# Optimization experiments

Hardware: AMD Instinct MI355X
Metric: run time of the kernel (lower is better)

The kernel has to match this reference:

```python
import jax, jax.numpy as jnp
import numpy as np


def sign_ste(x):
    # torch BNN Binarize: sign() applied to .data => forward sign, backward identity (STE)
    return x + jax.lax.stop_gradient(jnp.sign(x) - x)


def setup_inputs() -> dict:
    key = jax.random.key(0)
    ks = jax.random.split(key, 5)
    B = 65536
    return {
        "x": jax.random.normal(ks[0], (B, 1, 28, 28), dtype=jnp.float32),
        "w_conv": jax.random.normal(ks[1], (3, 1, 4, 4), dtype=jnp.float32) * 0.1,
        "b_conv": jax.random.normal(ks[2], (3,), dtype=jnp.float32) * 0.1,
        "w_fc": jax.random.normal(ks[3], (10, 1875), dtype=jnp.float32) * 0.05,
        "b_fc": jax.random.normal(ks[4], (10,), dtype=jnp.float32) * 0.05,
    }


def reference(x, w_conv, b_conv, w_fc, b_fc):
    # BinarizeConv2d(1,3,4): binarize input (in_ch=1 != 3) and weights, float bias
    xb = sign_ste(x)
    wcb = sign_ste(w_conv)
    y = jax.lax.conv_general_dilated(
        xb, wcb, window_strides=(1, 1), padding="VALID",
        dimension_numbers=("NCHW", "OIHW", "NCHW"))  # [B,3,25,25]
    y = y + b_conv[None, :, None, None]
    h = y.reshape(y.shape[0], -1)  # [B,1875]
    # BinarizeLinear(1875,10): binarize input (1875 != 784) and weights
    hb = sign_ste(h)
    wfb = sign_ste(w_fc)
    out = hb @ wfb.T + b_fc  # [B,10]
    return sign_ste(out)
```

## Files before the change

### kernel.cpp

```cpp
#include <hip/hip_runtime.h>
#include <stdint.h>

#define XWORDS (65536 * 28)

__device__ __forceinline__ void FA(uint32_t a, uint32_t b, uint32_t c,
                                   uint32_t& s, uint32_t& cy) {
  uint32_t ab = a ^ b;
  s = ab ^ c;
  cy = (a & b) | (ab & c);
}

__global__ __launch_bounds__(256) void pack_kernel(
    const float* __restrict__ x, const float* __restrict__ w_fc,
    uint32_t* __restrict__ xp, uint32_t* __restrict__ wfp)
{
  int t = blockIdx.x * 256 + threadIdx.x;
  if (t < XWORDS) {
    const float4* p = (const float4*)(x + (size_t)t * 28);
    uint32_t m = 0;
    #pragma unroll
    for (int q = 0; q < 7; ++q) {
      float4 v = p[q];
      m = (m >> 1) | (__float_as_uint(v.x) & 0x80000000u);
      m = (m >> 1) | (__float_as_uint(v.y) & 0x80000000u);
      m = (m >> 1) | (__float_as_uint(v.z) & 0x80000000u);
      m = (m >> 1) | (__float_as_uint(v.w) & 0x80000000u);
    }
    xp[t] = m >> 4;
  } else {
    int s = t - XWORDS;
    if (s < 750) {
      int ci = s / 10, k = s % 10;
      uint32_t m = 0;
      #pragma unroll
      for (int j = 0; j < 25; ++j)
        m |= (__float_as_uint(w_fc[k * 1875 + ci * 25 + j]) >> 31) << j;
      wfp[ci * 12 + k] = m;
    }
  }
}

__global__ __launch_bounds__(256) void bnn_main(
    const uint32_t* __restrict__ xp, const uint32_t* __restrict__ wfp,
    const float* __restrict__ w_conv, const float* __restrict__ b_conv,
    const float* __restrict__ b_fc, float* __restrict__ out)
{
  __shared__ __align__(16) uint32_t swf[900];
  __shared__ uint32_t srows[256 * 29];
  const int tid = threadIdx.x;
  const int b = blockIdx.x * 256 + tid;

  for (int i = tid; i < 900; i += 256) swf[i] = wfp[i];

  const uint4* rp = (const uint4*)(xp + (size_t)b * 28);
  uint32_t* my = &srows[tid * 29];
  #pragma unroll
  for (int q = 0; q < 7; ++q) {
    uint4 v = rp[q];
    my[q * 4 + 0] = v.x; my[q * 4 + 1] = v.y;
    my[q * 4 + 2] = v.z; my[q * 4 + 3] = v.w;
  }
  __syncthreads();

  uint32_t wm[3][16], sbc[3];
  #pragma unroll
  for (int c = 0; c < 3; ++c) {
    #pragma unroll
    for (int uv = 0; uv < 16; ++uv)
      wm[c][uv] = (uint32_t)((int32_t)__float_as_uint(w_conv[c * 16 + uv]) >> 31);
    sbc[c] = (uint32_t)((int32_t)__float_as_uint(b_conv[c]) >> 31);
  }

  int nd[10] = {0, 0, 0, 0, 0, 0, 0, 0, 0, 0};

  for (int i = 0; i < 25; ++i) {
    uint32_t r0 = my[i], r1 = my[i + 1], r2 = my[i + 2], r3 = my[i + 3];
    #pragma unroll
    for (int c = 0; c < 3; ++c) {
      const uint32_t* W = wm[c];
      uint32_t s0, c0, s1, c1, s2, c2, s3, c3, s4, c4;
      FA( r0 ^ W[0],        (r0 ^ W[1])  >> 1, (r0 ^ W[2])  >> 2, s0, c0);
      FA((r0 ^ W[3]) >> 3,   r1 ^ W[4],        (r1 ^ W[5])  >> 1, s1, c1);
      FA((r1 ^ W[6]) >> 2,  (r1 ^ W[7])  >> 3,  r2 ^ W[8],        s2, c2);
      FA((r2 ^ W[9]) >> 1,  (r2 ^ W[10]) >> 2, (r2 ^ W[11]) >> 3, s3, c3);
      FA( r3 ^ W[12],       (r3 ^ W[13]) >> 1, (r3 ^ W[14]) >> 2, s4, c4);
      uint32_t t15 = (r3 ^ W[15]) >> 3;
      uint32_t u0, d0, u1, d1;
      FA(s0, s1, s2, u0, d0); FA(s3, s4, t15, u1, d1);
      uint32_t bb0 = u0 ^ u1, e0 = u0 & u1;
      uint32_t p0, q0, p1, q1, p2, q2;
      FA(c0, c1, c2, p0, q0); FA(c3, c4, d0, p1, q1); FA(d1, e0, p0, p2, q2);
      uint32_t bb1 = p1 ^ p2, q3 = p1 & p2;
      uint32_t r0_, r1_;
      FA(q0, q1, q2, r0_, r1_);
      uint32_t bb2 = r0_ ^ q3, r2_ = r0_ & q3;
      uint32_t bb3 = r1_ ^ r2_, bb4 = r1_ & r2_;
      uint32_t low = bb0 | bb1 | bb2;
      uint32_t neg = (bb4 | (bb3 & (low | sbc[c]))) & 0x1FFFFFFu;
      int ci = c * 25 + i;
      uint4 wA = *(const uint4*)&swf[ci * 12];
      uint4 wB = *(const uint4*)&swf[ci * 12 + 4];
      uint2 wC = *(const uint2*)&swf[ci * 12 + 8];
      nd[0] += __popc(neg ^ wA.x); nd[1] += __popc(neg ^ wA.y);
      nd[2] += __popc(neg ^ wA.z); nd[3] += __popc(neg ^ wA.w);
      nd[4] += __popc(neg ^ wB.x); nd[5] += __popc(neg ^ wB.y);
      nd[6] += __popc(neg ^ wB.z); nd[7] += __popc(neg ^ wB.w);
      nd[8] += __popc(neg ^ wC.x); nd[9] += __popc(neg ^ wC.y);
    }
  }

  float* op = out + (size_t)b * 10;
  #pragma unroll
  for (int k = 0; k < 10; k += 2) {
    float v0 = (float)(1875 - 2 * nd[k])     + b_fc[k];
    float v1 = (float)(1875 - 2 * nd[k + 1]) + b_fc[k + 1];
    float2 st;
    st.x = v0 < 0.f ? -1.f : (v0 > 0.f ? 1.f : 0.f);
    st.y = v1 < 0.f ? -1.f : (v1 > 0.f ? 1.f : 0.f);
    *(float2*)(op + k) = st;
  }
}

extern "C" void kernel_launch(void* const* d_in, const int* in_sizes, int n_in,
                              void* d_out, int out_size, void* d_ws, size_t ws_size,
                              hipStream_t stream) {
  const float* x      = (const float*)d_in[0];
  const float* w_conv = (const float*)d_in[1];
  const float* b_conv = (const float*)d_in[2];
  const float* w_fc   = (const float*)d_in[3];
  const float* b_fc   = (const float*)d_in[4];

  uint32_t* xp  = (uint32_t*)d_ws;
  uint32_t* wfp = xp + XWORDS;

  pack_kernel<<<7171, 256, 0, stream>>>(x, w_fc, xp, wfp);
  bnn_main<<<256, 256, 0, stream>>>(xp, wfp, w_conv, b_conv, b_fc, (float*)d_out);
}
```

Before: 304.3 us.

## Fuse input packing into main kernel and split conv rows across four lanes

Merges the separate pack kernel into the main kernel. Each 256-thread block now loads 64 images with coalesced float4 reads, packs their sign bits into shared memory, and rebuilds 28-bit row masks. Each image's 25 output rows are split across 4 threads, with the partial popcounts combined by xor-shuffles. This removes the packed-input round trip through global memory and the second launch, and raises the grid from 256 blocks to 1024. The cost is that every block repacks the FC weights and the shuffles add a reduction step.

```diff
diff --git a/kernel.cpp b/kernel.cpp
--- a/kernel.cpp
+++ b/kernel.cpp
@@ -1,7 +1,8 @@
 #include <hip/hip_runtime.h>
 #include <stdint.h>
 
-#define XWORDS (65536 * 28)
+#define IMB 64
+#define NBLK (65536 / IMB)
 
 __device__ __forceinline__ void FA(uint32_t a, uint32_t b, uint32_t c,
                                    uint32_t& s, uint32_t& cy) {
@@ -10,72 +11,71 @@
   cy = (a & b) | (ab & c);
 }
 
-__global__ __launch_bounds__(256) void pack_kernel(
-    const float* __restrict__ x, const float* __restrict__ w_fc,
-    uint32_t* __restrict__ xp, uint32_t* __restrict__ wfp)
-{
-  int t = blockIdx.x * 256 + threadIdx.x;
-  if (t < XWORDS) {
-    const float4* p = (const float4*)(x + (size_t)t * 28);
-    uint32_t m = 0;
-    #pragma unroll
-    for (int q = 0; q < 7; ++q) {
-      float4 v = p[q];
-      m = (m >> 1) | (__float_as_uint(v.x) & 0x80000000u);
-      m = (m >> 1) | (__float_as_uint(v.y) & 0x80000000u);
-      m = (m >> 1) | (__float_as_uint(v.z) & 0x80000000u);
-      m = (m >> 1) | (__float_as_uint(v.w) & 0x80000000u);
-    }
-    xp[t] = m >> 4;
-  } else {
-    int s = t - XWORDS;
-    if (s < 750) {
-      int ci = s / 10, k = s % 10;
-      uint32_t m = 0;
-      #pragma unroll
-      for (int j = 0; j < 25; ++j)
-        m |= (__float_as_uint(w_fc[k * 1875 + ci * 25 + j]) >> 31) << j;
-      wfp[ci * 12 + k] = m;
-    }
-  }
-}
-
-__global__ __launch_bounds__(256) void bnn_main(
-    const uint32_t* __restrict__ xp, const uint32_t* __restrict__ wfp,
-    const float* __restrict__ w_conv, const float* __restrict__ b_conv,
+__global__ __launch_bounds__(256) void bnn_fused(
+    const float* __restrict__ x, const float* __restrict__ w_conv,
+    const float* __restrict__ b_conv, const float* __restrict__ w_fc,
     const float* __restrict__ b_fc, float* __restrict__ out)
 {
+  __shared__ uint8_t  nib[IMB * 196];
+  __shared__ uint32_t srows[IMB * 29];
   __shared__ __align__(16) uint32_t swf[900];
-  __shared__ uint32_t srows[256 * 29];
   const int tid = threadIdx.x;
-  const int b = blockIdx.x * 256 + tid;
-
-  for (int i = tid; i < 900; i += 256) swf[i] = wfp[i];
-
-  const uint4* rp = (const uint4*)(xp + (size_t)b * 28);
-  uint32_t* my = &srows[tid * 29];
-  #pragma unroll
-  for (int q = 0; q < 7; ++q) {
-    uint4 v = rp[q];
-    my[q * 4 + 0] = v.x; my[q * 4 + 1] = v.y;
-    my[q * 4 + 2] = v.z; my[q * 4 + 3] = v.w;
-  }
-  __syncthreads();
 
   uint32_t wm[3][16], sbc[3];
-  #pragma unroll
+#pragma unroll
   for (int c = 0; c < 3; ++c) {
-    #pragma unroll
+#pragma unroll
     for (int uv = 0; uv < 16; ++uv)
       wm[c][uv] = (uint32_t)((int32_t)__float_as_uint(w_conv[c * 16 + uv]) >> 31);
     sbc[c] = (uint32_t)((int32_t)__float_as_uint(b_conv[c]) >> 31);
   }
 
-  int nd[10] = {0, 0, 0, 0, 0, 0, 0, 0, 0, 0};
+  for (int s = tid; s < 750; s += 256) {
+    int ci = s / 10, k = s - ci * 10;
+    const float* wr = w_fc + k * 1875 + ci * 25;
+    uint32_t m = 0;
+#pragma unroll
+    for (int j = 0; j < 25; ++j)
+      m |= (__float_as_uint(wr[j]) >> 31) << j;
+    swf[ci * 12 + k] = m;
+  }
 
-  for (int i = 0; i < 25; ++i) {
+  const float4* xv = (const float4*)(x + (size_t)blockIdx.x * (IMB * 784));
+#pragma unroll 4
+  for (int q = 0; q < 49; ++q) {
+    int idx = q * 256 + tid;
+    float4 v = xv[idx];
+    uint32_t n = (__float_as_uint(v.x) >> 31)
+               | ((__float_as_uint(v.y) >> 31) << 1)
+               | ((__float_as_uint(v.z) >> 31) << 2)
+               | ((__float_as_uint(v.w) >> 31) << 3);
+    nib[idx] = (uint8_t)n;
+  }
+  __syncthreads();
+
+#pragma unroll
+  for (int q = 0; q < 7; ++q) {
+    int r = q * 256 + tid;
+    const uint8_t* p = &nib[r * 7];
+    uint32_t m = (uint32_t)p[0]        | ((uint32_t)p[1] << 4)
+               | ((uint32_t)p[2] << 8) | ((uint32_t)p[3] << 12)
+               | ((uint32_t)p[4] << 16)| ((uint32_t)p[5] << 20)
+               | ((uint32_t)p[6] << 24);
+    int mi = r / 28, rowin = r - mi * 28;
+    srows[mi * 29 + rowin] = m;
+  }
+  __syncthreads();
+
+  const int sub = tid & 3;
+  const int img = tid >> 2;
+  const uint32_t* my = &srows[img * 29];
+  int nd[10] = {0,0,0,0,0,0,0,0,0,0};
+  int ilo = sub * 7;
+  int ihi = ilo + 7; if (ihi > 25) ihi = 25;
+
+  for (int i = ilo; i < ihi; ++i) {
     uint32_t r0 = my[i], r1 = my[i + 1], r2 = my[i + 2], r3 = my[i + 3];
-    #pragma unroll
+#pragma unroll
     for (int c = 0; c < 3; ++c) {
       const uint32_t* W = wm[c];
       uint32_t s0, c0, s1, c1, s2, c2, s3, c3, s4, c4;
@@ -109,15 +109,23 @@
     }
   }
 
-  float* op = out + (size_t)b * 10;
-  #pragma unroll
-  for (int k = 0; k < 10; k += 2) {
-    float v0 = (float)(1875 - 2 * nd[k])     + b_fc[k];
-    float v1 = (float)(1875 - 2 * nd[k + 1]) + b_fc[k + 1];
-    float2 st;
-    st.x = v0 < 0.f ? -1.f : (v0 > 0.f ? 1.f : 0.f);
-    st.y = v1 < 0.f ? -1.f : (v1 > 0.f ? 1.f : 0.f);
-    *(float2*)(op + k) = st;
+#pragma unroll
+  for (int k = 0; k < 10; ++k) nd[k] += __shfl_xor(nd[k], 1);
+#pragma unroll
+  for (int k = 0; k < 10; ++k) nd[k] += __shfl_xor(nd[k], 2);
+
+  if (sub == 0) {
+    const size_t bi = (size_t)blockIdx.x * IMB + img;
+    float* op = out + bi * 10;
+#pragma unroll
+    for (int k = 0; k < 10; k += 2) {
+      float v0 = (float)(1875 - 2 * nd[k])     + b_fc[k];
+      float v1 = (float)(1875 - 2 * nd[k + 1]) + b_fc[k + 1];
+      float2 st;
+      st.x = v0 < 0.f ? -1.f : (v0 > 0.f ? 1.f : 0.f);
+      st.y = v1 < 0.f ? -1.f : (v1 > 0.f ? 1.f : 0.f);
+      *(float2*)(op + k) = st;
+    }
   }
 }
 
@@ -129,10 +137,6 @@
   const float* b_conv = (const float*)d_in[2];
   const float* w_fc   = (const float*)d_in[3];
   const float* b_fc   = (const float*)d_in[4];
-
-  uint32_t* xp  = (uint32_t*)d_ws;
-  uint32_t* wfp = xp + XWORDS;
-
-  pack_kernel<<<7171, 256, 0, stream>>>(x, w_fc, xp, wfp);
-  bnn_main<<<256, 256, 0, stream>>>(xp, wfp, w_conv, b_conv, b_fc, (float*)d_out);
+  bnn_fused<<<NBLK, 256, 0, stream>>>(x, w_conv, b_conv, w_fc, b_fc,
+                                      (float*)d_out);
 }
```

Result: no change. 303.7 us (-0.2%).
